# Performance work log

Measured on AMD Instinct MI355X. Metric: run time of the kernel, lower is better.

Reference implementation:

```python
import jax, jax.numpy as jnp
import numpy as np

B, S, D, H = 2, 2048, 1024, 16
HD = D // H  # head dim = 64


def setup_inputs() -> dict:
    key = jax.random.key(0)
    ks = jax.random.split(key, 8)
    s = 0.02
    return {
        "Q": jax.random.normal(ks[0], (B, S, D), jnp.float32),
        "K": jax.random.normal(ks[1], (B, S, D), jnp.float32),
        "V": jax.random.normal(ks[2], (B, S, D), jnp.float32),
        "mask": jax.random.randint(ks[3], (1, 1, S, S), 0, 2, jnp.int32),
        "Wq": jax.random.normal(ks[4], (D, D), jnp.float32) * s,
        "bq": jnp.zeros((D,), jnp.float32),
        "Wk": jax.random.normal(ks[5], (D, D), jnp.float32) * s,
        "bk": jnp.zeros((D,), jnp.float32),
        "Wv": jax.random.normal(ks[6], (D, D), jnp.float32) * s,
        "bv": jnp.zeros((D,), jnp.float32),
        "Wo": jax.random.normal(ks[7], (D, D), jnp.float32) * s,
        "bo": jnp.zeros((D,), jnp.float32),
    }


def reference(Q, K, V, mask, Wq, bq, Wk, bk, Wv, bv, Wo, bo):
    b = Q.shape[0]
    # QKV projections, split into heads: [B,S,D] -> [B,H,S,HD]
    q = (Q @ Wq + bq).reshape(b, -1, H, HD).transpose(0, 2, 1, 3)
    k = (K @ Wk + bk).reshape(b, -1, H, HD).transpose(0, 2, 1, 3)
    v = (V @ Wv + bv).reshape(b, -1, H, HD).transpose(0, 2, 1, 3)
    # scaled dot-product attention with full [B,H,S,S] scores (as in source)
    scale = jnp.sqrt(jnp.asarray(HD, q.dtype))
    scores = jnp.einsum("bhqd,bhkd->bhqk", q, k) / scale
    scores = jnp.where(mask == 0, -jnp.inf, scores)
    attn = jax.nn.softmax(scores, axis=-1)
    ctx = jnp.einsum("bhqk,bhkd->bhqd", attn, v)
    # merge heads and output projection
    concat = ctx.transpose(0, 2, 1, 3).reshape(b, -1, H * HD)
    return concat @ Wo + bo
```

## Files before the change

### kernel.cpp

```cpp
#include <hip/hip_runtime.h>


using s8v = __attribute__((ext_vector_type(8))) short;
using f4v = __attribute__((ext_vector_type(4))) float;
using f16v = __attribute__((ext_vector_type(16))) float;
typedef unsigned long long u64;

__device__ __forceinline__ unsigned short f2bf(float f) {
  union { float f; unsigned int u; } v; v.f = f;
  return (unsigned short)((v.u + 0x7fffu + ((v.u >> 16) & 1u)) >> 16);
}

__device__ __forceinline__ unsigned pkbf(float lo, float hi2) {
  return __builtin_amdgcn_perm(__float_as_uint(hi2), __float_as_uint(lo), 0x07060302);
}

__device__ __forceinline__ void gll16(const void* g, void* l) {
  __builtin_amdgcn_global_load_lds(
      (const __attribute__((address_space(1))) unsigned int*)g,
      (__attribute__((address_space(3))) unsigned int*)l, 16, 0, 0);
}

__global__ void prep_kernel(const float* __restrict__ Q, const float* __restrict__ K,
                            const float* __restrict__ V,
                            unsigned short* __restrict__ qb, unsigned short* __restrict__ kb,
                            unsigned short* __restrict__ vb,
                            const float* __restrict__ W0, const float* __restrict__ W1,
                            const float* __restrict__ W2, const float* __restrict__ W3,
                            unsigned short* __restrict__ T0, unsigned short* __restrict__ T1,
                            unsigned short* __restrict__ T2, unsigned short* __restrict__ T3,
                            const int* __restrict__ mask, u64* __restrict__ bm) {
  __shared__ unsigned short t[64][72];
  const int bid = blockIdx.x, tid = threadIdx.x;
  if (bid < 12288) {
    int z = bid >> 12;
    int idx = (bid & 4095) * 256 + tid;
    const float* in = (z == 0) ? Q : (z == 1) ? K : V;
    unsigned short* out = (z == 0) ? qb : (z == 1) ? kb : vb;
    float4 v = ((const float4*)in)[idx];
    ushort4 o;
    o.x = f2bf(v.x); o.y = f2bf(v.y); o.z = f2bf(v.z); o.w = f2bf(v.w);
    ((ushort4*)out)[idx] = o;
  } else if (bid < 13312) {
    int b = bid - 12288;
    int z = b >> 8, rem = b & 255;
    int k0 = (rem >> 4) * 64, n0 = (rem & 15) * 64;
    const float* W = (z == 0) ? W0 : (z == 1) ? W1 : (z == 2) ? W2 : W3;
    unsigned short* Wt = (z == 0) ? T0 : (z == 1) ? T1 : (z == 2) ? T2 : T3;
    for (int p = 0; p < 4; ++p) {
      int idx = p * 256 + tid;
      int row = idx >> 4, c4 = idx & 15;
      float4 v = *(const float4*)&W[(size_t)(k0 + row) * 1024 + n0 + c4 * 4];
      t[row][c4 * 4 + 0] = f2bf(v.x);
      t[row][c4 * 4 + 1] = f2bf(v.y);
      t[row][c4 * 4 + 2] = f2bf(v.z);
      t[row][c4 * 4 + 3] = f2bf(v.w);
    }
    __syncthreads();
    for (int p = 0; p < 2; ++p) {
      int idx = p * 256 + tid;
      int j = idx >> 3, c8 = idx & 7;
      unsigned short tmp[8];
      for (int i = 0; i < 8; ++i) tmp[i] = t[c8 * 8 + i][j];
      uint4 o;
      o.x = tmp[0] | ((unsigned)tmp[1] << 16);
      o.y = tmp[2] | ((unsigned)tmp[3] << 16);
      o.z = tmp[4] | ((unsigned)tmp[5] << 16);
      o.w = tmp[6] | ((unsigned)tmp[7] << 16);
      *(uint4*)&Wt[(size_t)(n0 + j) * 1024 + k0 + c8 * 8] = o;
    }
  } else {
    int b = bid - 13312;
    int gw = (b * 256 + tid) >> 6;
    int lane = tid & 63;
    int mv = mask[(size_t)gw * 64 + lane];
    u64 bal = __ballot(mv != 0);
    if (lane == 0) bm[gw] = bal;
  }
}

__global__ __launch_bounds__(256) void proj3_kernel(
    const unsigned short* __restrict__ A0, const unsigned short* __restrict__ A1,
    const unsigned short* __restrict__ A2,
    const unsigned short* __restrict__ W0, const unsigned short* __restrict__ W1,
    const unsigned short* __restrict__ W2,
    const float* __restrict__ b0, const float* __restrict__ b1, const float* __restrict__ b2,
    unsigned short* __restrict__ oq, unsigned short* __restrict__ ok,
    unsigned short* __restrict__ ovt) {
  const int z = blockIdx.z;
  const unsigned short* A  = (z == 0) ? A0 : (z == 1) ? A1 : A2;
  const unsigned short* Wt = (z == 0) ? W0 : (z == 1) ? W1 : W2;
  const float* bias        = (z == 0) ? b0 : (z == 1) ? b1 : b2;

  __shared__ __align__(16) unsigned short As[64 * 32];
  __shared__ __align__(16) unsigned short Bs[128 * 32];

  const int tid = threadIdx.x;
  const int lane = tid & 63, w = tid >> 6, ln = lane & 15, quad = lane >> 4;
  const int wm = (w & 1) * 32, wn = (w >> 1) * 64;
  const int m0 = blockIdx.x * 64, n0 = blockIdx.y * 128;

  const int slr = lane >> 2;
  const int schunk = (lane & 3) ^ ((lane >> 3) & 3);
  const int cfrag = (quad ^ ((ln >> 1) & 3)) * 8;

  f4v zero = {0.f, 0.f, 0.f, 0.f};
  f4v acc[2][4];
  for (int mi = 0; mi < 2; ++mi)
    for (int ni = 0; ni < 4; ++ni) acc[mi][ni] = zero;

  for (int kt = 0; kt < 1024; kt += 32) {
    __syncthreads();
    gll16(&A[(size_t)(m0 + w * 16 + slr) * 1024 + kt + schunk * 8],        &As[(w * 16) * 32]);
    gll16(&Wt[(size_t)(n0 + w * 32 + slr) * 1024 + kt + schunk * 8],       &Bs[(w * 32) * 32]);
    gll16(&Wt[(size_t)(n0 + w * 32 + 16 + slr) * 1024 + kt + schunk * 8],  &Bs[(w * 32 + 16) * 32]);
    __syncthreads();
    s8v a[2], b[4];
    for (int mi = 0; mi < 2; ++mi) a[mi] = *(const s8v*)&As[(wm + mi * 16 + ln) * 32 + cfrag];
    for (int ni = 0; ni < 4; ++ni) b[ni] = *(const s8v*)&Bs[(wn + ni * 16 + ln) * 32 + cfrag];
    if (z < 2) {
      for (int mi = 0; mi < 2; ++mi)
        for (int ni = 0; ni < 4; ++ni)
          acc[mi][ni] = __builtin_amdgcn_mfma_f32_16x16x32_bf16(a[mi], b[ni], acc[mi][ni], 0, 0, 0);
    } else {
      for (int mi = 0; mi < 2; ++mi)
        for (int ni = 0; ni < 4; ++ni)
          acc[mi][ni] = __builtin_amdgcn_mfma_f32_16x16x32_bf16(b[ni], a[mi], acc[mi][ni], 0, 0, 0);
    }
  }

  if (z < 2) {
    const float qscale = (z == 0) ? 0.18033688f : 1.0f;
    unsigned short* outp = (z == 0) ? oq : ok;
    for (int mi = 0; mi < 2; ++mi) {
      int rb = m0 + wm + mi * 16 + quad * 4;
      int b_ = rb >> 11;
      for (int ni = 0; ni < 4; ++ni) {
        int col = n0 + wn + ni * 16 + ln;
        float bvv = bias[col];
        int h = col >> 6, hd = col & 63;
        size_t ob = (size_t)(b_ * 16 + h) * 2048;
        for (int r = 0; r < 4; ++r) {
          int s = (rb + r) & 2047;
          outp[(ob + s) * 64 + hd] = f2bf((acc[mi][ni][r] + bvv) * qscale);
        }
      }
    }
  } else {
    for (int ni = 0; ni < 4; ++ni) {
      for (int r = 0; r < 4; ++r) {
        int colw = n0 + wn + ni * 16 + quad * 4 + r;
        int h = colw >> 6, hd = colw & 63;
        float bvv = bias[colw];
        for (int mi = 0; mi < 2; ++mi) {
          int sg = m0 + wm + mi * 16 + ln;
          int b_ = sg >> 11, ss = sg & 2047;
          ovt[((size_t)(b_ * 16 + h) * 64 + hd) * 2048 + ss] = f2bf(acc[mi][ni][r] + bvv);
        }
      }
    }
  }
}

__global__ __launch_bounds__(256) void flash_kernel(
    const unsigned short* __restrict__ q, const unsigned short* __restrict__ k,
    const unsigned short* __restrict__ vt, const u64* __restrict__ bm,
    unsigned short* __restrict__ ctx) {
  __shared__ __align__(16) unsigned short k_s[2][64][72];
  __shared__ __align__(16) unsigned short v_s[2][64][72];

  const int tid = threadIdx.x;
  const int lane = tid & 63, w = tid >> 6;
  const int l31 = lane & 31, hi = lane >> 5;
  const int q0 = blockIdx.x * 128;
  const int bh = blockIdx.y;
  const unsigned short* qg  = q  + ((size_t)bh * 2048 + q0) * 64;
  const unsigned short* kgb = k  + (size_t)bh * 2048 * 64;
  const unsigned short* vgb = vt + (size_t)bh * 64 * 2048;

  const int qrow = w * 32 + l31;
  s8v qf[4];
#pragma unroll
  for (int c = 0; c < 4; ++c)
    qf[c] = *(const s8v*)&qg[(size_t)qrow * 64 + c * 16 + hi * 8];

  const u64* bmr = bm + (size_t)(q0 + qrow) * 32;

  s8v ones;
#pragma unroll
  for (int i = 0; i < 8; ++i) ones[i] = (short)0x3F80;

  const int srow = tid >> 3, sc8 = tid & 7;

  uint4 kr0 = *(const uint4*)&kgb[(size_t)srow * 64 + sc8 * 8];
  uint4 kr1 = *(const uint4*)&kgb[(size_t)(srow + 32) * 64 + sc8 * 8];
  uint4 vr0 = *(const uint4*)&vgb[(size_t)srow * 2048 + sc8 * 8];
  uint4 vr1 = *(const uint4*)&vgb[(size_t)(srow + 32) * 2048 + sc8 * 8];
  *(uint4*)&k_s[0][srow][sc8 * 8] = kr0;
  *(uint4*)&k_s[0][srow + 32][sc8 * 8] = kr1;
  *(uint4*)&v_s[0][srow][sc8 * 8] = vr0;
  *(uint4*)&v_s[0][srow + 32][sc8 * 8] = vr1;
  kr0 = *(const uint4*)&kgb[(size_t)(64 + srow) * 64 + sc8 * 8];
  kr1 = *(const uint4*)&kgb[(size_t)(64 + srow + 32) * 64 + sc8 * 8];
  vr0 = *(const uint4*)&vgb[(size_t)srow * 2048 + 64 + sc8 * 8];
  vr1 = *(const uint4*)&vgb[(size_t)(srow + 32) * 2048 + 64 + sc8 * 8];
  __syncthreads();

  f16v o0, o1, lac;
#pragma unroll
  for (int i = 0; i < 16; ++i) { o0[i] = 0.f; o1[i] = 0.f; lac[i] = 0.f; }

  for (int kt = 0; kt < 2048; kt += 64) {
    const int cur = (kt >> 6) & 1;
    u64 mwc = bmr[kt >> 6];

    if (kt + 64 < 2048) {
      const int nxt = cur ^ 1;
      *(uint4*)&k_s[nxt][srow][sc8 * 8] = kr0;
      *(uint4*)&k_s[nxt][srow + 32][sc8 * 8] = kr1;
      *(uint4*)&v_s[nxt][srow][sc8 * 8] = vr0;
      *(uint4*)&v_s[nxt][srow + 32][sc8 * 8] = vr1;
      if (kt + 128 < 2048) {
        const int kn = kt + 128;
        kr0 = *(const uint4*)&kgb[(size_t)(kn + srow) * 64 + sc8 * 8];
        kr1 = *(const uint4*)&kgb[(size_t)(kn + srow + 32) * 64 + sc8 * 8];
        vr0 = *(const uint4*)&vgb[(size_t)srow * 2048 + kn + sc8 * 8];
        vr1 = *(const uint4*)&vgb[(size_t)(srow + 32) * 2048 + kn + sc8 * 8];
      }
    }

    f16v s0, s1;
#pragma unroll
    for (int i = 0; i < 16; ++i) { s0[i] = 0.f; s1[i] = 0.f; }
#pragma unroll
    for (int c = 0; c < 4; ++c) {
      s8v ak0 = *(const s8v*)&k_s[cur][l31][c * 16 + hi * 8];
      s8v ak1 = *(const s8v*)&k_s[cur][32 + l31][c * 16 + hi * 8];
      s0 = __builtin_amdgcn_mfma_f32_32x32x16_bf16(ak0, qf[c], s0, 0, 0, 0);
      s1 = __builtin_amdgcn_mfma_f32_32x32x16_bf16(ak1, qf[c], s1, 0, 0, 0);
    }

    const u64 mq = mwc >> (4 * hi);
    s8v pf[4];
#pragma unroll
    for (int ni = 0; ni < 2; ++ni) {
      const unsigned half = (unsigned)(mq >> (32 * ni));
      float p[16];
#pragma unroll
      for (int g = 0; g < 4; ++g) {
        const unsigned nib = (half >> (8 * g)) & 0xFu;
#pragma unroll
        for (int m = 0; m < 4; ++m) {
          const float sv = (ni ? s1[g * 4 + m] : s0[g * 4 + m]);
          p[g * 4 + m] = __builtin_amdgcn_exp2f(sv) * (float)((nib >> m) & 1u);
        }
      }
#pragma unroll
      for (int kcl = 0; kcl < 2; ++kcl) {
        const int rb = 8 * kcl;
        unsigned x0 = pkbf(p[rb + 0], p[rb + 1]);
        unsigned x1 = pkbf(p[rb + 2], p[rb + 3]);
        unsigned y0 = pkbf(p[rb + 4], p[rb + 5]);
        unsigned y1 = pkbf(p[rb + 6], p[rb + 7]);
        asm("v_permlane32_swap_b32 %0, %1" : "+v"(x0), "+v"(y0));
        asm("v_permlane32_swap_b32 %0, %1" : "+v"(x1), "+v"(y1));
        union { uint4 u; s8v v; } cv;
        cv.u = make_uint4(x0, x1, y0, y1);
        pf[ni * 2 + kcl] = cv.v;
      }
    }

#pragma unroll
    for (int kc = 0; kc < 4; ++kc)
      lac = __builtin_amdgcn_mfma_f32_32x32x16_bf16(pf[kc], ones, lac, 0, 0, 0);

#pragma unroll
    for (int kc = 0; kc < 4; ++kc) {
      s8v bv0 = *(const s8v*)&v_s[cur][l31][kc * 16 + hi * 8];
      s8v bv1 = *(const s8v*)&v_s[cur][32 + l31][kc * 16 + hi * 8];
      o0 = __builtin_amdgcn_mfma_f32_32x32x16_bf16(pf[kc], bv0, o0, 0, 0, 0);
      o1 = __builtin_amdgcn_mfma_f32_32x32x16_bf16(pf[kc], bv1, o1, 0, 0, 0);
    }
    __syncthreads();
  }

  const int b_ = bh >> 4, h = bh & 15;
#pragma unroll
  for (int r = 0; r < 16; ++r) {
    const int ql = (r & 3) + 8 * (r >> 2) + 4 * hi;
    const float inv = 1.f / lac[r];
    const int srw = q0 + w * 32 + ql;
    const size_t base = ((size_t)b_ * 2048 + srw) * 1024 + h * 64;
    ctx[base + l31] = f2bf(o0[r] * inv);
    ctx[base + 32 + l31] = f2bf(o1[r] * inv);
  }
}

__global__ __launch_bounds__(256) void gemm_out_kernel(
    const unsigned short* __restrict__ A, const unsigned short* __restrict__ Wt,
    const float* __restrict__ bias, float* __restrict__ out) {
  __shared__ __align__(16) unsigned short As[64 * 32];
  __shared__ __align__(16) unsigned short Bs[128 * 32];

  const int tid = threadIdx.x;
  const int lane = tid & 63, w = tid >> 6, ln = lane & 15, quad = lane >> 4;
  const int wm = (w & 1) * 32, wn = (w >> 1) * 64;
  const int m0 = blockIdx.x * 64, n0 = blockIdx.y * 128;

  const int slr = lane >> 2;
  const int schunk = (lane & 3) ^ ((lane >> 3) & 3);
  const int cfrag = (quad ^ ((ln >> 1) & 3)) * 8;

  f4v zero = {0.f, 0.f, 0.f, 0.f};
  f4v acc[2][4];
  for (int mi = 0; mi < 2; ++mi)
    for (int ni = 0; ni < 4; ++ni) acc[mi][ni] = zero;

  for (int kt = 0; kt < 1024; kt += 32) {
    __syncthreads();
    gll16(&A[(size_t)(m0 + w * 16 + slr) * 1024 + kt + schunk * 8],        &As[(w * 16) * 32]);
    gll16(&Wt[(size_t)(n0 + w * 32 + slr) * 1024 + kt + schunk * 8],       &Bs[(w * 32) * 32]);
    gll16(&Wt[(size_t)(n0 + w * 32 + 16 + slr) * 1024 + kt + schunk * 8],  &Bs[(w * 32 + 16) * 32]);
    __syncthreads();
    s8v a[2], b[4];
    for (int mi = 0; mi < 2; ++mi) a[mi] = *(const s8v*)&As[(wm + mi * 16 + ln) * 32 + cfrag];
    for (int ni = 0; ni < 4; ++ni) b[ni] = *(const s8v*)&Bs[(wn + ni * 16 + ln) * 32 + cfrag];
    for (int mi = 0; mi < 2; ++mi)
      for (int ni = 0; ni < 4; ++ni)
        acc[mi][ni] = __builtin_amdgcn_mfma_f32_16x16x32_bf16(a[mi], b[ni], acc[mi][ni], 0, 0, 0);
  }

  for (int mi = 0; mi < 2; ++mi) {
    int rb = m0 + wm + mi * 16 + quad * 4;
    for (int ni = 0; ni < 4; ++ni) {
      int col = n0 + wn + ni * 16 + ln;
      float bvv = bias[col];
      for (int r = 0; r < 4; ++r)
        out[(size_t)(rb + r) * 1024 + col] = acc[mi][ni][r] + bvv;
    }
  }
}

extern "C" void kernel_launch(void* const* d_in, const int* in_sizes, int n_in,
                              void* d_out, int out_size, void* d_ws, size_t ws_size,
                              hipStream_t stream) {
  const float* Q  = (const float*)d_in[0];
  const float* K  = (const float*)d_in[1];
  const float* V  = (const float*)d_in[2];
  const int* mask = (const int*)d_in[3];
  const float* Wq = (const float*)d_in[4];
  const float* bq = (const float*)d_in[5];
  const float* Wk = (const float*)d_in[6];
  const float* bk = (const float*)d_in[7];
  const float* Wv = (const float*)d_in[8];
  const float* bv = (const float*)d_in[9];
  const float* Wo = (const float*)d_in[10];
  const float* bo = (const float*)d_in[11];
  float* out = (float*)d_out;

  char* ws = (char*)d_ws;
  const size_t MB = 1u << 20;
  unsigned short* qb  = (unsigned short*)(ws + 0 * MB);
  unsigned short* kb  = (unsigned short*)(ws + 8 * MB);
  unsigned short* vb  = (unsigned short*)(ws + 16 * MB);
  unsigned short* wqt = (unsigned short*)(ws + 24 * MB);
  unsigned short* wkt = (unsigned short*)(ws + 26 * MB);
  unsigned short* wvt = (unsigned short*)(ws + 28 * MB);
  unsigned short* wot = (unsigned short*)(ws + 30 * MB);
  unsigned short* qh  = (unsigned short*)(ws + 32 * MB);
  unsigned short* kh  = (unsigned short*)(ws + 40 * MB);
  unsigned short* vth = (unsigned short*)(ws + 48 * MB);
  u64* bm             = (u64*)(ws + 56 * MB);
  unsigned short* ctx = (unsigned short*)(ws + 16 * MB);

  prep_kernel<<<29696, 256, 0, stream>>>(Q, K, V, qb, kb, vb,
                                         Wq, Wk, Wv, Wo, wqt, wkt, wvt, wot,
                                         mask, bm);
  proj3_kernel<<<dim3(64, 8, 3), 256, 0, stream>>>(qb, kb, vb, wqt, wkt, wvt,
                                                   bq, bk, bv, qh, kh, vth);
  flash_kernel<<<dim3(16, 32), 256, 0, stream>>>(qh, kh, vth, bm, ctx);
  gemm_out_kernel<<<dim3(64, 8), 256, 0, stream>>>(ctx, wot, bo, out);
}
```

Before: 264.0 us.

## Precompute mask as per-lane bf16 AND-words laid out to match MFMA fragments

The mask preprocessing now writes 32-bit AND masks (0xFFFF per allowed element), ordered to match each lane's packed bf16 P fragment layout. The flash kernel loads four uint4 per tile and ANDs them into the packed probabilities, which removes the per-element bit extraction, float conversion and multiply after exp2. It also adds s_setprio around MFMA blocks and launch_bounds occupancy hint 2. The cost is a mask buffer 16x larger (read per tile from global memory) and extra memory traffic, while the prep grid shrinks.

Result: faster. 247.3 us (-6.3%).

```diff
diff --git a/kernel.cpp b/kernel.cpp
--- a/kernel.cpp
+++ b/kernel.cpp
@@ -29,7 +29,7 @@
                             const float* __restrict__ W2, const float* __restrict__ W3,
                             unsigned short* __restrict__ T0, unsigned short* __restrict__ T1,
                             unsigned short* __restrict__ T2, unsigned short* __restrict__ T3,
-                            const int* __restrict__ mask, u64* __restrict__ bm) {
+                            const int* __restrict__ mask, unsigned* __restrict__ bmw) {
   __shared__ unsigned short t[64][72];
   const int bid = blockIdx.x, tid = threadIdx.x;
   if (bid < 12288) {
@@ -70,12 +70,15 @@
       *(uint4*)&Wt[(size_t)(n0 + j) * 1024 + k0 + c8 * 8] = o;
     }
   } else {
-    int b = bid - 13312;
-    int gw = (b * 256 + tid) >> 6;
-    int lane = tid & 63;
-    int mv = mask[(size_t)gw * 64 + lane];
-    u64 bal = __ballot(mv != 0);
-    if (lane == 0) bm[gw] = bal;
+    int g = (bid - 13312) * 256 + tid;
+    int widx = g & 15, hi = (g >> 4) & 1, l31 = (g >> 5) & 31;
+    int it = (g >> 10) & 31, rowblk = g >> 15;
+    int ni = widx >> 3, kcl = (widx >> 2) & 1, e = widx & 3;
+    int kk = 64 * it + 32 * ni + 16 * kcl + 4 * hi + (e >> 1) * 8 + (e & 1) * 2;
+    int qrow = rowblk * 32 + l31;
+    const int* mrow = mask + (size_t)qrow * 2048 + kk;
+    unsigned wd = (mrow[0] ? 0xFFFFu : 0u) | (mrow[1] ? 0xFFFF0000u : 0u);
+    bmw[g] = wd;
   }
 }
 
@@ -162,9 +165,9 @@
   }
 }
 
-__global__ __launch_bounds__(256) void flash_kernel(
+__global__ __launch_bounds__(256, 2) void flash_kernel(
     const unsigned short* __restrict__ q, const unsigned short* __restrict__ k,
-    const unsigned short* __restrict__ vt, const u64* __restrict__ bm,
+    const unsigned short* __restrict__ vt, const unsigned* __restrict__ bmw,
     unsigned short* __restrict__ ctx) {
   __shared__ __align__(16) unsigned short k_s[2][64][72];
   __shared__ __align__(16) unsigned short v_s[2][64][72];
@@ -177,6 +180,7 @@
   const unsigned short* qg  = q  + ((size_t)bh * 2048 + q0) * 64;
   const unsigned short* kgb = k  + (size_t)bh * 2048 * 64;
   const unsigned short* vgb = vt + (size_t)bh * 64 * 2048;
+  const unsigned* mwp = bmw + (size_t)(blockIdx.x * 4 + w) * 32768 + l31 * 32 + hi * 16;
 
   const int qrow = w * 32 + l31;
   s8v qf[4];
@@ -184,11 +188,12 @@
   for (int c = 0; c < 4; ++c)
     qf[c] = *(const s8v*)&qg[(size_t)qrow * 64 + c * 16 + hi * 8];
 
-  const u64* bmr = bm + (size_t)(q0 + qrow) * 32;
-
   s8v ones;
 #pragma unroll
   for (int i = 0; i < 8; ++i) ones[i] = (short)0x3F80;
+  f16v zf;
+#pragma unroll
+  for (int i = 0; i < 16; ++i) zf[i] = 0.f;
 
   const int srow = tid >> 3, sc8 = tid & 7;
 
@@ -212,7 +217,8 @@
 
   for (int kt = 0; kt < 2048; kt += 64) {
     const int cur = (kt >> 6) & 1;
-    u64 mwc = bmr[kt >> 6];
+    const uint4* mw4 = (const uint4*)(mwp + (kt >> 6) * 1024);
+    const uint4 mwA = mw4[0], mwB = mw4[1], mwC = mw4[2], mwD = mw4[3];
 
     if (kt + 64 < 2048) {
       const int nxt = cur ^ 1;
@@ -229,39 +235,35 @@
       }
     }
 
-    f16v s0, s1;
-#pragma unroll
-    for (int i = 0; i < 16; ++i) { s0[i] = 0.f; s1[i] = 0.f; }
-#pragma unroll
-    for (int c = 0; c < 4; ++c) {
-      s8v ak0 = *(const s8v*)&k_s[cur][l31][c * 16 + hi * 8];
-      s8v ak1 = *(const s8v*)&k_s[cur][32 + l31][c * 16 + hi * 8];
+    __builtin_amdgcn_s_setprio(1);
+    s8v ak0 = *(const s8v*)&k_s[cur][l31][hi * 8];
+    s8v ak1 = *(const s8v*)&k_s[cur][32 + l31][hi * 8];
+    f16v s0 = __builtin_amdgcn_mfma_f32_32x32x16_bf16(ak0, qf[0], zf, 0, 0, 0);
+    f16v s1 = __builtin_amdgcn_mfma_f32_32x32x16_bf16(ak1, qf[0], zf, 0, 0, 0);
+#pragma unroll
+    for (int c = 1; c < 4; ++c) {
+      ak0 = *(const s8v*)&k_s[cur][l31][c * 16 + hi * 8];
+      ak1 = *(const s8v*)&k_s[cur][32 + l31][c * 16 + hi * 8];
       s0 = __builtin_amdgcn_mfma_f32_32x32x16_bf16(ak0, qf[c], s0, 0, 0, 0);
       s1 = __builtin_amdgcn_mfma_f32_32x32x16_bf16(ak1, qf[c], s1, 0, 0, 0);
     }
-
-    const u64 mq = mwc >> (4 * hi);
+    __builtin_amdgcn_s_setprio(0);
+
     s8v pf[4];
 #pragma unroll
     for (int ni = 0; ni < 2; ++ni) {
-      const unsigned half = (unsigned)(mq >> (32 * ni));
       float p[16];
 #pragma unroll
-      for (int g = 0; g < 4; ++g) {
-        const unsigned nib = (half >> (8 * g)) & 0xFu;
-#pragma unroll
-        for (int m = 0; m < 4; ++m) {
-          const float sv = (ni ? s1[g * 4 + m] : s0[g * 4 + m]);
-          p[g * 4 + m] = __builtin_amdgcn_exp2f(sv) * (float)((nib >> m) & 1u);
-        }
-      }
+      for (int i = 0; i < 16; ++i)
+        p[i] = __builtin_amdgcn_exp2f(ni ? s1[i] : s0[i]);
 #pragma unroll
       for (int kcl = 0; kcl < 2; ++kcl) {
         const int rb = 8 * kcl;
-        unsigned x0 = pkbf(p[rb + 0], p[rb + 1]);
-        unsigned x1 = pkbf(p[rb + 2], p[rb + 3]);
-        unsigned y0 = pkbf(p[rb + 4], p[rb + 5]);
-        unsigned y1 = pkbf(p[rb + 6], p[rb + 7]);
+        const uint4 mw = ni ? (kcl ? mwD : mwC) : (kcl ? mwB : mwA);
+        unsigned x0 = pkbf(p[rb + 0], p[rb + 1]) & mw.x;
+        unsigned x1 = pkbf(p[rb + 2], p[rb + 3]) & mw.y;
+        unsigned y0 = pkbf(p[rb + 4], p[rb + 5]) & mw.z;
+        unsigned y1 = pkbf(p[rb + 6], p[rb + 7]) & mw.w;
         asm("v_permlane32_swap_b32 %0, %1" : "+v"(x0), "+v"(y0));
         asm("v_permlane32_swap_b32 %0, %1" : "+v"(x1), "+v"(y1));
         union { uint4 u; s8v v; } cv;
@@ -270,10 +272,10 @@
       }
     }
 
+    __builtin_amdgcn_s_setprio(1);
 #pragma unroll
     for (int kc = 0; kc < 4; ++kc)
       lac = __builtin_amdgcn_mfma_f32_32x32x16_bf16(pf[kc], ones, lac, 0, 0, 0);
-
 #pragma unroll
     for (int kc = 0; kc < 4; ++kc) {
       s8v bv0 = *(const s8v*)&v_s[cur][l31][kc * 16 + hi * 8];
@@ -281,6 +283,7 @@
       o0 = __builtin_amdgcn_mfma_f32_32x32x16_bf16(pf[kc], bv0, o0, 0, 0, 0);
       o1 = __builtin_amdgcn_mfma_f32_32x32x16_bf16(pf[kc], bv1, o1, 0, 0, 0);
     }
+    __builtin_amdgcn_s_setprio(0);
     __syncthreads();
   }
 
@@ -370,14 +373,14 @@
   unsigned short* qh  = (unsigned short*)(ws + 32 * MB);
   unsigned short* kh  = (unsigned short*)(ws + 40 * MB);
   unsigned short* vth = (unsigned short*)(ws + 48 * MB);
-  u64* bm             = (u64*)(ws + 56 * MB);
+  unsigned* bmw       = (unsigned*)(ws + 56 * MB);
   unsigned short* ctx = (unsigned short*)(ws + 16 * MB);
 
-  prep_kernel<<<29696, 256, 0, stream>>>(Q, K, V, qb, kb, vb,
+  prep_kernel<<<21504, 256, 0, stream>>>(Q, K, V, qb, kb, vb,
                                          Wq, Wk, Wv, Wo, wqt, wkt, wvt, wot,
-                                         mask, bm);
+                                         mask, bmw);
   proj3_kernel<<<dim3(64, 8, 3), 256, 0, stream>>>(qb, kb, vb, wqt, wkt, wvt,
                                                    bq, bk, bv, qh, kh, vth);
-  flash_kernel<<<dim3(16, 32), 256, 0, stream>>>(qh, kh, vth, bm, ctx);
+  flash_kernel<<<dim3(16, 32), 256, 0, stream>>>(qh, kh, vth, bmw, ctx);
   gemm_out_kernel<<<dim3(64, 8), 256, 0, stream>>>(ctx, wot, bo, out);
 }
```
